# Kernel optimization log

Hardware: AMD Instinct MI355X
Metric: run time of the kernel (lower is better)

Reference implementation:

```python
import jax, jax.numpy as jnp
import numpy as np


def _maxpool3d(x, s=2):
    # MaxPool3d(kernel_size=s) -> stride=s, VALID padding
    return jax.lax.reduce_window(x, -jnp.inf, jax.lax.max,
                                 (1, 1, s, s, s), (1, 1, s, s, s), 'VALID')


def _spectral_norm(W, u):
    # W: [out_c, in_c]. One power iteration with u/v detached, matching
    # torch.nn.utils.spectral_norm's training-step behavior.
    v = W.T @ u
    v = v / (jnp.linalg.norm(v) + 1e-12)
    u2 = W @ v
    u2 = u2 / (jnp.linalg.norm(u2) + 1e-12)
    u2 = jax.lax.stop_gradient(u2)
    v = jax.lax.stop_gradient(v)
    sigma = u2 @ (W @ v)
    return W / sigma


def setup_inputs() -> dict:
    key = jax.random.key(0)
    ks = jax.random.split(key, 6)
    B, C, D = 4, 256, 32
    kc, vc, oc = 128, 128, 256
    return {
        'x':  jax.random.normal(ks[0], (B, C, D, D, D), jnp.float32),
        'Wk': jax.random.normal(ks[1], (kc, C), jnp.float32) * 0.05,  # shared f_key/f_query 1x1x1 conv
        'bk': jnp.zeros((kc,), jnp.float32),
        'Wv': jax.random.normal(ks[2], (vc, C), jnp.float32) * 0.05,  # f_value 1x1x1 conv
        'bv': jnp.zeros((vc,), jnp.float32),
        'Ww': jax.random.normal(ks[3], (oc, vc), jnp.float32) * 0.05,  # output W 1x1x1 conv
        'bw': jnp.zeros((oc,), jnp.float32),
        'u':  jax.random.normal(ks[4], (kc,), jnp.float32),            # spectral-norm power-iter vector
    }


def reference(x, Wk, bk, Wv, bv, Ww, bw, u):
    B, C = x.shape[0], x.shape[1]
    kc = Wk.shape[0]
    xp = _maxpool3d(x, 2)                      # [B,C,16,16,16]
    sp = xp.shape[2:]
    N = sp[0] * sp[1] * sp[2]                  # 4096 flattened positions
    xf = xp.reshape(B, C, N)                   # [B,C,N]

    Wq = _spectral_norm(Wk, u)                 # f_query = f_key (shared weights)
    q = jnp.einsum('kc,bcn->bnk', Wq, xf) + bk                    # [B,N,kc]
    k = jnp.einsum('kc,bcn->bkn', Wq, xf) + bk[None, :, None]     # [B,kc,N]
    v = jnp.einsum('vc,bcn->bnv', Wv, xf) + bv                    # [B,N,vc]

    sim = jnp.einsum('bnk,bkm->bnm', q, k) * (kc ** -0.5)         # [B,N,N]
    attn = jax.nn.softmax(sim, axis=-1)
    ctx = jnp.einsum('bnm,bmv->bnv', attn, v)                     # [B,N,vc]

    out = jnp.einsum('ov,bnv->bon', Ww, ctx) + bw[None, :, None]  # [B,oc,N]
    return out.reshape(B, Ww.shape[0], *sp)    # [B,oc,16,16,16] (pooled spatial, as in original)
```

## Files before the change

kernel.cpp:

```cpp
#include <hip/hip_runtime.h>

typedef __attribute__((ext_vector_type(8))) short short8;
typedef __attribute__((ext_vector_type(4))) float f32x4;

static constexpr size_t OFF_SIGMA = 0;
static constexpr size_t OFF_ML    = 256;
static constexpr size_t OFF_QKT   = 1048576;
static constexpr size_t OFF_V     = OFF_QKT + 4194304;
static constexpr size_t OFF_WCAT  = OFF_V + 4194304;
static constexpr size_t OFF_XFB   = OFF_WCAT + 196608;
static constexpr size_t OFF_PC    = OFF_XFB;

__device__ inline unsigned short f2bf(float f) {
  unsigned int u = __float_as_uint(f);
  unsigned int r = u + 0x7fffu + ((u >> 16) & 1u);
  return (unsigned short)(r >> 16);
}
__device__ inline float bf2f(unsigned short s) {
  return __uint_as_float(((unsigned int)s) << 16);
}

__launch_bounds__(256)
__global__ void k_maxpool(const float* __restrict__ x, unsigned short* __restrict__ xfb) {
  int idx = blockIdx.x * 256 + threadIdx.x;
  int n2 = idx & 2047;
  int bc = idx >> 11;
  int d2p = n2 & 7, d1 = (n2 >> 3) & 15, d0 = n2 >> 7;
  const float* p = x + (size_t)bc * 32768 + (size_t)d0 * 2048 + d1 * 64 + d2p * 4;
  float4 a = *(const float4*)(p);
  float4 b = *(const float4*)(p + 32);
  float4 c = *(const float4*)(p + 1024);
  float4 e = *(const float4*)(p + 1056);
  float o0 = fmaxf(fmaxf(fmaxf(a.x, a.y), fmaxf(b.x, b.y)),
                   fmaxf(fmaxf(c.x, c.y), fmaxf(e.x, e.y)));
  float o1 = fmaxf(fmaxf(fmaxf(a.z, a.w), fmaxf(b.z, b.w)),
                   fmaxf(fmaxf(c.z, c.w), fmaxf(e.z, e.w)));
  unsigned int pk = (unsigned int)f2bf(o0) | ((unsigned int)f2bf(o1) << 16);
  *(unsigned int*)(xfb + (size_t)bc * 4096 + n2 * 2) = pk;
}

__global__ void k_sigma(const float* __restrict__ Wk, const float* __restrict__ u,
                        float* __restrict__ sig) {
  __shared__ float vsh[256];
  __shared__ float red[256];
  __shared__ float ush[128];
  int t = threadIdx.x;
  if (t < 128) ush[t] = u[t];
  __syncthreads();
  float acc = 0.f;
  for (int k = 0; k < 128; k++) acc += Wk[(size_t)k * 256 + t] * ush[k];
  vsh[t] = acc;
  red[t] = acc * acc;
  __syncthreads();
  for (int s = 128; s > 0; s >>= 1) { if (t < s) red[t] += red[t + s]; __syncthreads(); }
  float nrm = sqrtf(red[0]) + 1e-12f;
  float vn = vsh[t] / nrm;
  __syncthreads();
  vsh[t] = vn;
  __syncthreads();
  float acc2 = 0.f;
  if (t < 128) {
    for (int c = 0; c < 256; c++) acc2 += Wk[(size_t)t * 256 + c] * vsh[c];
  }
  red[t] = (t < 128) ? acc2 * acc2 : 0.f;
  __syncthreads();
  for (int s = 128; s > 0; s >>= 1) { if (t < s) red[t] += red[t + s]; __syncthreads(); }
  if (t == 0) {
    float s2v = red[0];
    sig[0] = s2v / (sqrtf(s2v) + 1e-12f);
  }
}

__launch_bounds__(256)
__global__ void k_prep(const float* __restrict__ Ww, const float* __restrict__ Wk,
                       const float* __restrict__ Wv, unsigned short* __restrict__ wcat) {
  int i = (blockIdx.x * 256 + threadIdx.x) * 4;
  const float* src = (i < 32768) ? (Ww + i) : (i < 65536) ? (Wk + i - 32768)
                                                          : (Wv + i - 65536);
  float4 w = *(const float4*)src;
  unsigned int lo = (unsigned int)f2bf(w.x) | ((unsigned int)f2bf(w.y) << 16);
  unsigned int hi = (unsigned int)f2bf(w.z) | ((unsigned int)f2bf(w.w) << 16);
  *(uint2*)(wcat + i) = make_uint2(lo, hi);
}

__launch_bounds__(256)
__global__ void k_qkv(const unsigned short* __restrict__ xfb,
                      const unsigned short* __restrict__ wcat,
                      const float* __restrict__ bk, const float* __restrict__ bv,
                      const float* __restrict__ sig,
                      unsigned short* __restrict__ qkT, unsigned short* __restrict__ vws) {
  __shared__ __align__(16) unsigned short Bl[64 * 64];
  int bid = blockIdx.x;
  int nt = bid & 63, b = bid >> 6;
  int n0 = nt * 64;
  int t = threadIdx.x, wid = t >> 6, lane = t & 63, g = lane >> 4, lr = lane & 15;
  int R0 = wid * 64;
  bool isq = (wid < 2);
  const unsigned short* wb = isq ? (wcat + 32768 + (size_t)R0 * 256)
                                 : (wcat + 65536 + (size_t)(R0 - 128) * 256);
  f32x4 acc[4][4];
#pragma unroll
  for (int i = 0; i < 4; i++)
#pragma unroll
    for (int j = 0; j < 4; j++) acc[i][j] = (f32x4){0.f, 0.f, 0.f, 0.f};

  short8 st[2];
#pragma unroll
  for (int i = 0; i < 2; i++) {
    int gid = i * 256 + t;
    st[i] = *(const short8*)(xfb + ((size_t)(b * 256 + (gid >> 3))) * 4096 +
                             n0 + (gid & 7) * 8);
  }

#pragma unroll 1
  for (int ks4 = 0; ks4 < 4; ks4++) {
    int k0 = ks4 * 64;
    __syncthreads();
#pragma unroll
    for (int i = 0; i < 2; i++) {
      int gid = i * 256 + t;
      int c = gid >> 3, nch = gid & 7;
#pragma unroll
      for (int j = 0; j < 8; j++) {
        int n = nch * 8 + j;
        Bl[n * 64 + (((c >> 3) ^ (n & 7)) << 3) + (c & 7)] = (unsigned short)st[i][j];
      }
    }
    if (ks4 < 3) {
#pragma unroll
      for (int i = 0; i < 2; i++) {
        int gid = i * 256 + t;
        st[i] = *(const short8*)(xfb + ((size_t)(b * 256 + k0 + 64 + (gid >> 3))) * 4096 +
                                 n0 + (gid & 7) * 8);
      }
    }
    __syncthreads();
#pragma unroll
    for (int ks2 = 0; ks2 < 2; ks2++) {
      short8 af[4], bf[4];
#pragma unroll
      for (int ot = 0; ot < 4; ot++)
        af[ot] = *(const short8*)(wb + (size_t)(ot * 16 + lr) * 256 + k0 + ks2 * 32 + g * 8);
#pragma unroll
      for (int nt2 = 0; nt2 < 4; nt2++) {
        int n = nt2 * 16 + lr;
        bf[nt2] = *(const short8*)(Bl + n * 64 + (((ks2 * 4 + g) ^ (n & 7)) << 3));
      }
#pragma unroll
      for (int ot = 0; ot < 4; ot++)
#pragma unroll
        for (int nt2 = 0; nt2 < 4; nt2++)
          acc[ot][nt2] = __builtin_amdgcn_mfma_f32_16x16x32_bf16(af[ot], bf[nt2],
                                                                 acc[ot][nt2], 0, 0, 0);
    }
  }

  if (isq) {
    float inv_s = 1.0f / sig[0];
#pragma unroll
    for (int ot = 0; ot < 4; ot++)
#pragma unroll
      for (int rr = 0; rr < 4; rr++) {
        int d = R0 + ot * 16 + g * 4 + rr;
        float bias = bk[d];
#pragma unroll
        for (int nt2 = 0; nt2 < 4; nt2++) {
          int n = n0 + nt2 * 16 + lr;
          float val = acc[ot][nt2][rr] * inv_s + bias;
          int ds = ((((d >> 3) ^ (n & 7)) & 15) << 3) | (d & 7);
          qkT[((size_t)b * 4096 + n) * 128 + ds] = f2bf(val);
        }
      }
  } else {
#pragma unroll
    for (int ot = 0; ot < 4; ot++)
#pragma unroll
      for (int rr = 0; rr < 4; rr++) {
        int d = R0 - 128 + ot * 16 + g * 4 + rr;
        float bias = bv[d];
#pragma unroll
        for (int nt2 = 0; nt2 < 4; nt2++) {
          int n = n0 + nt2 * 16 + lr;
          int c = n & 63;
          int cs = ((((c >> 3) ^ (d & 7)) & 7) << 3) | (c & 7);
          vws[((size_t)(b * 128 + d)) * 4096 + (n & ~63) + cs] =
              f2bf(acc[ot][nt2][rr] + bias);
        }
      }
  }
}

__launch_bounds__(256, 2)
__global__ void k_attn(const unsigned short* __restrict__ qkT,
                       const unsigned short* __restrict__ vws,
                       unsigned short* __restrict__ pc, float* __restrict__ lsum) {
  __shared__ __align__(16) char smem[16384 + 16384 + 4 * 4608];
  const float C1 = 0.12751744f;
  int p = blockIdx.x;
  int bid = (p & 7) * 128 + (p >> 3);
  int sp = bid & 7, qt = (bid >> 3) & 31, b = bid >> 8;
  int kv0 = sp * 512;
  int t = threadIdx.x, wid = t >> 6, lane = t & 63, g = lane >> 4, lr = lane & 15;
  int qrb = qt * 128 + wid * 32;
  const unsigned short* qk_b = qkT + (size_t)b * 524288;
  const char* kgb = (const char*)qk_b;
  const char* vgb = (const char*)(vws + (size_t)b * 524288);
  char* KL = smem;
  char* VL = smem + 16384;
  unsigned short* PL = (unsigned short*)(smem + 32768 + wid * 4608);

  short8 qf[2][4];
#pragma unroll
  for (int rt = 0; rt < 2; rt++)
#pragma unroll
    for (int kk = 0; kk < 4; kk++) {
      int row = qrb + rt * 16 + lr;
      qf[rt][kk] = *(const short8*)(qk_b + (size_t)row * 128 +
                                    ((((kk * 4 + g) ^ (lr & 7)) & 15) << 3));
    }

  f32x4 cacc[2][8];
#pragma unroll
  for (int rt = 0; rt < 2; rt++)
#pragma unroll
    for (int vt = 0; vt < 8; vt++) cacc[rt][vt] = (f32x4){0.f, 0.f, 0.f, 0.f};
  float l0[4] = {0.f, 0.f, 0.f, 0.f}, l1[4] = {0.f, 0.f, 0.f, 0.f};

  int drow = t >> 3;
  int cb   = (t & 7) * 16;

  short8 kst[4], vst[4];
  {
    const char* kg = kgb + (size_t)kv0 * 256;
#pragma unroll
    for (int i = 0; i < 4; i++) kst[i] = *(const short8*)(kg + i * 4096 + t * 16);
#pragma unroll
    for (int i = 0; i < 4; i++)
      vst[i] = *(const short8*)(vgb + (size_t)(i * 32 + drow) * 8192 + kv0 * 2 + cb);
  }

#pragma unroll 1
  for (int it = 0; it < 8; ++it) {
    int mbase = kv0 + it * 64;
    __syncthreads();
#pragma unroll
    for (int i = 0; i < 4; i++) *(short8*)(KL + i * 4096 + t * 16) = kst[i];
#pragma unroll
    for (int i = 0; i < 4; i++) *(short8*)(VL + i * 4096 + t * 16) = vst[i];
    if (it < 7) {
      int mb = mbase + 64;
      const char* kg = kgb + (size_t)mb * 256;
#pragma unroll
      for (int i = 0; i < 4; i++) kst[i] = *(const short8*)(kg + i * 4096 + t * 16);
#pragma unroll
      for (int i = 0; i < 4; i++)
        vst[i] = *(const short8*)(vgb + (size_t)(i * 32 + drow) * 8192 + mb * 2 + cb);
    }
    __syncthreads();

#pragma unroll
    for (int ct = 0; ct < 4; ct++) {
      short8 kf[4];
#pragma unroll
      for (int kk = 0; kk < 4; kk++)
        kf[kk] = *(const short8*)(KL + (ct * 16 + lr) * 256 +
                                  ((((kk * 4 + g) ^ (lr & 7)) & 15) << 4));
      f32x4 a0 = {0.f, 0.f, 0.f, 0.f}, a1 = a0;
      __builtin_amdgcn_s_setprio(1);
#pragma unroll
      for (int kk = 0; kk < 4; kk++) {
        a0 = __builtin_amdgcn_mfma_f32_16x16x32_bf16(qf[0][kk], kf[kk], a0, 0, 0, 0);
        a1 = __builtin_amdgcn_mfma_f32_16x16x32_bf16(qf[1][kk], kf[kk], a1, 0, 0, 0);
      }
      __builtin_amdgcn_s_setprio(0);
#pragma unroll
      for (int r = 0; r < 4; r++) {
        float p0 = __builtin_amdgcn_exp2f(a0[r] * C1);
        float p1 = __builtin_amdgcn_exp2f(a1[r] * C1);
        l0[r] += p0;
        l1[r] += p1;
        PL[(g * 4 + r) * 72 + ct * 16 + lr] =
            (unsigned short)((__float_as_uint(p0) + 0x8000u) >> 16);
        PL[(16 + g * 4 + r) * 72 + ct * 16 + lr] =
            (unsigned short)((__float_as_uint(p1) + 0x8000u) >> 16);
      }
    }

    __builtin_amdgcn_s_setprio(1);
#pragma unroll
    for (int ks = 0; ks < 2; ks++) {
      short8 pa0 = *(const short8*)(PL + lr * 72 + ks * 32 + g * 8);
      short8 pa1 = *(const short8*)(PL + (16 + lr) * 72 + ks * 32 + g * 8);
#pragma unroll
      for (int vt = 0; vt < 8; vt++) {
        short8 vb = *(const short8*)(VL + (vt * 16 + lr) * 128 +
                                     ((((ks * 4 + g) ^ (lr & 7)) & 7) << 4));
        cacc[0][vt] = __builtin_amdgcn_mfma_f32_16x16x32_bf16(pa0, vb, cacc[0][vt], 0, 0, 0);
        cacc[1][vt] = __builtin_amdgcn_mfma_f32_16x16x32_bf16(pa1, vb, cacc[1][vt], 0, 0, 0);
      }
    }
    __builtin_amdgcn_s_setprio(0);
  }

#pragma unroll
  for (int r = 0; r < 4; r++) {
    float v = l0[r];
    v += __shfl_xor(v, 1); v += __shfl_xor(v, 2);
    v += __shfl_xor(v, 4); v += __shfl_xor(v, 8);
    l0[r] = v;
    float w = l1[r];
    w += __shfl_xor(w, 1); w += __shfl_xor(w, 2);
    w += __shfl_xor(w, 4); w += __shfl_xor(w, 8);
    l1[r] = w;
  }

  int rowrd = lane >> 4;
  int colrd = (lane & 15) * 8;
#pragma unroll
  for (int rt = 0; rt < 2; rt++) {
#pragma unroll
    for (int vt = 0; vt < 8; vt++)
#pragma unroll
      for (int r = 0; r < 4; r++)
        PL[(g * 4 + r) * 136 + vt * 16 + lr] =
            f2bf(rt ? cacc[1][vt][r] : cacc[0][vt][r]);
#pragma unroll
    for (int rnd = 0; rnd < 4; rnd++) {
      int row = rnd * 4 + rowrd;
      short8 v = *(const short8*)(PL + row * 136 + colrd);
      int n = qrb + rt * 16 + row;
      *(short8*)(pc + ((size_t)sp * 16384 + (size_t)b * 4096 + n) * 128 + colrd) = v;
    }
  }
  if (lr == 0) {
#pragma unroll
    for (int rt = 0; rt < 2; rt++)
#pragma unroll
      for (int r = 0; r < 4; r++) {
        int n = qrb + rt * 16 + g * 4 + r;
        lsum[sp * 16384 + (size_t)b * 4096 + n] = rt ? l1[r] : l0[r];
      }
  }
}

__launch_bounds__(256)
__global__ void k_mergeout(const unsigned short* __restrict__ pc,
                           const float* __restrict__ lsum,
                           const unsigned short* __restrict__ wwb,
                           const float* __restrict__ bw,
                           float* __restrict__ out) {
  __shared__ float inv_l[64];
  __shared__ __align__(16) unsigned short Bl[64 * 128];
  int bid = blockIdx.x;
  int nt = bid & 63, b = bid >> 6;
  int n0 = nt * 64;
  size_t gnb = (size_t)b * 4096 + n0;
  int t = threadIdx.x;

  if (t < 64) {
    float L = 0.f;
#pragma unroll
    for (int sp = 0; sp < 8; sp++) L += lsum[sp * 16384 + gnb + t];
    inv_l[t] = 1.f / L;
  }
  __syncthreads();

  {
    int n = t & 63, vs = t >> 6;
    float o[32] = {};
#pragma unroll
    for (int sp = 0; sp < 8; sp++) {
      const unsigned short* src = pc + ((size_t)sp * 16384 + gnb + n) * 128 + vs * 32;
#pragma unroll
      for (int c = 0; c < 4; c++) {
        short8 pv = *(const short8*)(src + c * 8);
#pragma unroll
        for (int j = 0; j < 8; j++) o[c * 8 + j] += bf2f((unsigned short)pv[j]);
      }
    }
    float inv = inv_l[n];
    unsigned int* B32 = (unsigned int*)Bl;
#pragma unroll
    for (int jj = 0; jj < 16; jj++) {
      int v = vs * 32 + jj * 2;
      int kg = v >> 3;
      int kgp = (kg & 8) | ((kg ^ n) & 7);
      unsigned int pk = (unsigned int)f2bf(o[jj * 2] * inv) |
                        ((unsigned int)f2bf(o[jj * 2 + 1] * inv) << 16);
      B32[n * 64 + kgp * 4 + ((v & 7) >> 1)] = pk;
    }
  }
  __syncthreads();

  int wid = t >> 6, lane = t & 63, g = lane >> 4, lr = lane & 15;
  int o0 = wid * 64;
  short8 af[4][4];
#pragma unroll
  for (int ot = 0; ot < 4; ot++) {
    int o = o0 + ot * 16 + lr;
#pragma unroll
    for (int ks = 0; ks < 4; ks++)
      af[ot][ks] = *(const short8*)(wwb + (size_t)o * 128 + ks * 32 + g * 8);
  }
  f32x4 acc[4][4];
#pragma unroll
  for (int i = 0; i < 4; i++)
#pragma unroll
    for (int j = 0; j < 4; j++) acc[i][j] = (f32x4){0.f, 0.f, 0.f, 0.f};
#pragma unroll
  for (int nt2 = 0; nt2 < 4; nt2++) {
    short8 bfr[4];
#pragma unroll
    for (int ks = 0; ks < 4; ks++) {
      int kg = ks * 4 + g;
      int kgp = (kg & 8) | ((kg ^ lr) & 7);
      bfr[ks] = *(const short8*)(Bl + (nt2 * 16 + lr) * 128 + kgp * 8);
    }
#pragma unroll
    for (int ot = 0; ot < 4; ot++)
#pragma unroll
      for (int ks = 0; ks < 4; ks++)
        acc[ot][nt2] = __builtin_amdgcn_mfma_f32_16x16x32_bf16(af[ot][ks], bfr[ks],
                                                               acc[ot][nt2], 0, 0, 0);
  }
#pragma unroll
  for (int ot = 0; ot < 4; ot++)
#pragma unroll
    for (int r = 0; r < 4; r++) {
      int o = o0 + ot * 16 + g * 4 + r;
      float bias = bw[o];
#pragma unroll
      for (int nt2 = 0; nt2 < 4; nt2++)
        out[((size_t)(b * 256 + o)) * 4096 + n0 + nt2 * 16 + lr] = acc[ot][nt2][r] + bias;
    }
}

extern "C" void kernel_launch(void* const* d_in, const int* in_sizes, int n_in,
                              void* d_out, int out_size, void* d_ws, size_t ws_size,
                              hipStream_t stream) {
  const float* x  = (const float*)d_in[0];
  const float* Wk = (const float*)d_in[1];
  const float* bk = (const float*)d_in[2];
  const float* Wv = (const float*)d_in[3];
  const float* bv = (const float*)d_in[4];
  const float* Ww = (const float*)d_in[5];
  const float* bw = (const float*)d_in[6];
  const float* u  = (const float*)d_in[7];

  char* ws = (char*)d_ws;
  float* sig            = (float*)(ws + OFF_SIGMA);
  float* lsum           = (float*)(ws + OFF_ML);
  unsigned short* qkT   = (unsigned short*)(ws + OFF_QKT);
  unsigned short* vbuf  = (unsigned short*)(ws + OFF_V);
  unsigned short* wcat  = (unsigned short*)(ws + OFF_WCAT);
  unsigned short* xfb   = (unsigned short*)(ws + OFF_XFB);
  unsigned short* pc    = (unsigned short*)(ws + OFF_PC);
  float* out            = (float*)d_out;

  k_maxpool<<<8192, 256, 0, stream>>>(x, xfb);
  k_sigma<<<1, 256, 0, stream>>>(Wk, u, sig);
  k_prep<<<96, 256, 0, stream>>>(Ww, Wk, Wv, wcat);
  k_qkv<<<256, 256, 0, stream>>>(xfb, wcat, bk, bv, sig, qkT, vbuf);
  k_attn<<<1024, 256, 0, stream>>>(qkT, vbuf, pc, lsum);
  k_mergeout<<<256, 256, 0, stream>>>(pc, lsum, wcat, bw, out);
}
```

Measured before the change: 107.9 us.

## Rewrite attention inner loop with 32x32 MFMA, direct LDS loads and register-resident P

The attention kernel moves from 16x16x32 to 32x32x16 bf16 MFMA and computes S transposed (K as the A operand), so the probabilities come out in registers already laid out for the PV matmul. They are packed with v_cvt_pk_bf16 and permlane32_swap, which removes the per-wave LDS round trip for P. K/V tiles are staged with global_load_lds into a double-buffered 64KB shared array, replacing the register-staged copies and one of the two barriers per iteration. The larger LDS footprint may limit occupancy, and the output layout and rounding mode change.

After: 109.6 us. No clear change (+1.6%).

```diff
diff --git a/kernel.cpp b/kernel.cpp
--- a/kernel.cpp
+++ b/kernel.cpp
@@ -2,6 +2,7 @@
 
 typedef __attribute__((ext_vector_type(8))) short short8;
 typedef __attribute__((ext_vector_type(4))) float f32x4;
+typedef __attribute__((ext_vector_type(16))) float f32x16;
 
 static constexpr size_t OFF_SIGMA = 0;
 static constexpr size_t OFF_ML    = 256;
@@ -18,6 +19,11 @@
 }
 __device__ inline float bf2f(unsigned short s) {
   return __uint_as_float(((unsigned int)s) << 16);
+}
+__device__ inline unsigned int cvtpk_bf16(float a, float b) {
+  unsigned int r;
+  asm("v_cvt_pk_bf16_f32 %0, %1, %2" : "=v"(r) : "v"(a), "v"(b));
+  return r;
 }
 
 __launch_bounds__(256)
@@ -194,153 +200,151 @@
 __global__ void k_attn(const unsigned short* __restrict__ qkT,
                        const unsigned short* __restrict__ vws,
                        unsigned short* __restrict__ pc, float* __restrict__ lsum) {
-  __shared__ __align__(16) char smem[16384 + 16384 + 4 * 4608];
+  __shared__ __align__(16) char smem[2][32768];
   const float C1 = 0.12751744f;
   int p = blockIdx.x;
   int bid = (p & 7) * 128 + (p >> 3);
   int sp = bid & 7, qt = (bid >> 3) & 31, b = bid >> 8;
   int kv0 = sp * 512;
-  int t = threadIdx.x, wid = t >> 6, lane = t & 63, g = lane >> 4, lr = lane & 15;
+  int t = threadIdx.x, wid = t >> 6, lane = t & 63;
+  int l31 = lane & 31, hi = lane >> 5;
   int qrb = qt * 128 + wid * 32;
   const unsigned short* qk_b = qkT + (size_t)b * 524288;
   const char* kgb = (const char*)qk_b;
   const char* vgb = (const char*)(vws + (size_t)b * 524288);
-  char* KL = smem;
-  char* VL = smem + 16384;
-  unsigned short* PL = (unsigned short*)(smem + 32768 + wid * 4608);
-
-  short8 qf[2][4];
-#pragma unroll
-  for (int rt = 0; rt < 2; rt++)
-#pragma unroll
-    for (int kk = 0; kk < 4; kk++) {
-      int row = qrb + rt * 16 + lr;
-      qf[rt][kk] = *(const short8*)(qk_b + (size_t)row * 128 +
-                                    ((((kk * 4 + g) ^ (lr & 7)) & 15) << 3));
-    }
-
-  f32x4 cacc[2][8];
-#pragma unroll
-  for (int rt = 0; rt < 2; rt++)
-#pragma unroll
-    for (int vt = 0; vt < 8; vt++) cacc[rt][vt] = (f32x4){0.f, 0.f, 0.f, 0.f};
-  float l0[4] = {0.f, 0.f, 0.f, 0.f}, l1[4] = {0.f, 0.f, 0.f, 0.f};
-
-  int drow = t >> 3;
-  int cb   = (t & 7) * 16;
-
-  short8 kst[4], vst[4];
+
+  bool stk = (wid < 2);
+  int ch0 = (wid & 1) * 8;
+  const char* vsrc_base = vgb + (size_t)(lane >> 3) * 8192 + (lane & 7) * 16;
+
+#define STAGE(BUF, MB)                                                         \
+  {                                                                            \
+    char* base_ = smem[BUF];                                                   \
+    _Pragma("unroll")                                                          \
+    for (int i_ = 0; i_ < 8; i_++) {                                           \
+      int ch_ = ch0 + i_;                                                      \
+      if (stk) {                                                               \
+        const char* g_ = kgb + (size_t)(MB) * 256 + ch_ * 1024 + lane * 16;    \
+        __builtin_amdgcn_global_load_lds(                                      \
+            (const __attribute__((address_space(1))) unsigned int*)g_,         \
+            (__attribute__((address_space(3))) unsigned int*)(base_ + ch_ * 1024), \
+            16, 0, 0);                                                         \
+      } else {                                                                 \
+        const char* g_ = vsrc_base + (size_t)ch_ * 65536 + (size_t)(MB) * 2;   \
+        __builtin_amdgcn_global_load_lds(                                      \
+            (const __attribute__((address_space(1))) unsigned int*)g_,         \
+            (__attribute__((address_space(3))) unsigned int*)(base_ + 16384 + ch_ * 1024), \
+            16, 0, 0);                                                         \
+      }                                                                        \
+    }                                                                          \
+  }
+
+  STAGE(0, kv0)
+
+  short8 qf[8];
   {
-    const char* kg = kgb + (size_t)kv0 * 256;
-#pragma unroll
-    for (int i = 0; i < 4; i++) kst[i] = *(const short8*)(kg + i * 4096 + t * 16);
-#pragma unroll
-    for (int i = 0; i < 4; i++)
-      vst[i] = *(const short8*)(vgb + (size_t)(i * 32 + drow) * 8192 + kv0 * 2 + cb);
-  }
+    int row = qrb + l31;
+    const unsigned short* qr = qk_b + (size_t)row * 128;
+#pragma unroll
+    for (int kk = 0; kk < 8; kk++)
+      qf[kk] = *(const short8*)(qr + (((2 * kk + hi) ^ (row & 7)) << 3));
+  }
+
+  f32x16 acc[4];
+#pragma unroll
+  for (int dt = 0; dt < 4; dt++)
+#pragma unroll
+    for (int r = 0; r < 16; r++) acc[dt][r] = 0.f;
+  float lacc = 0.f;
+
+  __syncthreads();
 
 #pragma unroll 1
   for (int it = 0; it < 8; ++it) {
-    int mbase = kv0 + it * 64;
+    int cur = it & 1;
+    if (it < 7) STAGE(cur ^ 1, kv0 + it * 64 + 64)
+    const char* KL = smem[cur];
+    const char* VL = smem[cur] + 16384;
+
+    f32x16 s0, s1;
+#pragma unroll
+    for (int r = 0; r < 16; r++) { s0[r] = 0.f; s1[r] = 0.f; }
+    __builtin_amdgcn_s_setprio(1);
+#pragma unroll
+    for (int kk = 0; kk < 8; kk++) {
+      int cs = 2 * kk + hi;
+      short8 kf0 = *(const short8*)(KL + l31 * 256 + ((cs ^ (l31 & 7)) << 4));
+      short8 kf1 = *(const short8*)(KL + (32 + l31) * 256 + ((cs ^ (l31 & 7)) << 4));
+      s0 = __builtin_amdgcn_mfma_f32_32x32x16_bf16(kf0, qf[kk], s0, 0, 0, 0);
+      s1 = __builtin_amdgcn_mfma_f32_32x32x16_bf16(kf1, qf[kk], s1, 0, 0, 0);
+    }
+    __builtin_amdgcn_s_setprio(0);
+
+    short8 pa[4];
+#pragma unroll
+    for (int ct = 0; ct < 2; ct++) {
+      unsigned int w0[4], w1[4];
+#pragma unroll
+      for (int a = 0; a < 4; a++) {
+        float v0 = ct ? s1[4 * a + 0] : s0[4 * a + 0];
+        float v1 = ct ? s1[4 * a + 1] : s0[4 * a + 1];
+        float v2 = ct ? s1[4 * a + 2] : s0[4 * a + 2];
+        float v3 = ct ? s1[4 * a + 3] : s0[4 * a + 3];
+        float p0 = __builtin_amdgcn_exp2f(v0 * C1);
+        float p1 = __builtin_amdgcn_exp2f(v1 * C1);
+        float p2 = __builtin_amdgcn_exp2f(v2 * C1);
+        float p3 = __builtin_amdgcn_exp2f(v3 * C1);
+        lacc += (p0 + p1) + (p2 + p3);
+        w0[a] = cvtpk_bf16(p0, p1);
+        w1[a] = cvtpk_bf16(p2, p3);
+      }
+#pragma unroll
+      for (int k2 = 0; k2 < 2; k2++) {
+        unsigned int xa = w0[2 * k2], ya = w0[2 * k2 + 1];
+        unsigned int xb = w1[2 * k2], yb = w1[2 * k2 + 1];
+        asm("v_permlane32_swap_b32 %0, %1" : "+v"(xa), "+v"(ya));
+        asm("v_permlane32_swap_b32 %0, %1" : "+v"(xb), "+v"(yb));
+        union { unsigned int u[4]; short8 s8; } pk_;
+        pk_.u[0] = xa; pk_.u[1] = xb; pk_.u[2] = ya; pk_.u[3] = yb;
+        pa[ct * 2 + k2] = pk_.s8;
+      }
+    }
+
+    __builtin_amdgcn_s_setprio(1);
+#pragma unroll
+    for (int ks = 0; ks < 4; ks++) {
+      int cv = 2 * ks + hi;
+#pragma unroll
+      for (int dt = 0; dt < 4; dt++) {
+        int d = dt * 32 + l31;
+        short8 vb = *(const short8*)(VL + d * 128 + ((cv ^ (d & 7)) << 4));
+        acc[dt] = __builtin_amdgcn_mfma_f32_32x32x16_bf16(pa[ks], vb, acc[dt], 0, 0, 0);
+      }
+    }
+    __builtin_amdgcn_s_setprio(0);
     __syncthreads();
-#pragma unroll
-    for (int i = 0; i < 4; i++) *(short8*)(KL + i * 4096 + t * 16) = kst[i];
-#pragma unroll
-    for (int i = 0; i < 4; i++) *(short8*)(VL + i * 4096 + t * 16) = vst[i];
-    if (it < 7) {
-      int mb = mbase + 64;
-      const char* kg = kgb + (size_t)mb * 256;
-#pragma unroll
-      for (int i = 0; i < 4; i++) kst[i] = *(const short8*)(kg + i * 4096 + t * 16);
-#pragma unroll
-      for (int i = 0; i < 4; i++)
-        vst[i] = *(const short8*)(vgb + (size_t)(i * 32 + drow) * 8192 + mb * 2 + cb);
-    }
-    __syncthreads();
-
-#pragma unroll
-    for (int ct = 0; ct < 4; ct++) {
-      short8 kf[4];
-#pragma unroll
-      for (int kk = 0; kk < 4; kk++)
-        kf[kk] = *(const short8*)(KL + (ct * 16 + lr) * 256 +
-                                  ((((kk * 4 + g) ^ (lr & 7)) & 15) << 4));
-      f32x4 a0 = {0.f, 0.f, 0.f, 0.f}, a1 = a0;
-      __builtin_amdgcn_s_setprio(1);
-#pragma unroll
-      for (int kk = 0; kk < 4; kk++) {
-        a0 = __builtin_amdgcn_mfma_f32_16x16x32_bf16(qf[0][kk], kf[kk], a0, 0, 0, 0);
-        a1 = __builtin_amdgcn_mfma_f32_16x16x32_bf16(qf[1][kk], kf[kk], a1, 0, 0, 0);
-      }
-      __builtin_amdgcn_s_setprio(0);
-#pragma unroll
-      for (int r = 0; r < 4; r++) {
-        float p0 = __builtin_amdgcn_exp2f(a0[r] * C1);
-        float p1 = __builtin_amdgcn_exp2f(a1[r] * C1);
-        l0[r] += p0;
-        l1[r] += p1;
-        PL[(g * 4 + r) * 72 + ct * 16 + lr] =
-            (unsigned short)((__float_as_uint(p0) + 0x8000u) >> 16);
-        PL[(16 + g * 4 + r) * 72 + ct * 16 + lr] =
-            (unsigned short)((__float_as_uint(p1) + 0x8000u) >> 16);
-      }
-    }
-
-    __builtin_amdgcn_s_setprio(1);
-#pragma unroll
-    for (int ks = 0; ks < 2; ks++) {
-      short8 pa0 = *(const short8*)(PL + lr * 72 + ks * 32 + g * 8);
-      short8 pa1 = *(const short8*)(PL + (16 + lr) * 72 + ks * 32 + g * 8);
-#pragma unroll
-      for (int vt = 0; vt < 8; vt++) {
-        short8 vb = *(const short8*)(VL + (vt * 16 + lr) * 128 +
-                                     ((((ks * 4 + g) ^ (lr & 7)) & 7) << 4));
-        cacc[0][vt] = __builtin_amdgcn_mfma_f32_16x16x32_bf16(pa0, vb, cacc[0][vt], 0, 0, 0);
-        cacc[1][vt] = __builtin_amdgcn_mfma_f32_16x16x32_bf16(pa1, vb, cacc[1][vt], 0, 0, 0);
-      }
-    }
-    __builtin_amdgcn_s_setprio(0);
-  }
-
-#pragma unroll
-  for (int r = 0; r < 4; r++) {
-    float v = l0[r];
-    v += __shfl_xor(v, 1); v += __shfl_xor(v, 2);
-    v += __shfl_xor(v, 4); v += __shfl_xor(v, 8);
-    l0[r] = v;
-    float w = l1[r];
-    w += __shfl_xor(w, 1); w += __shfl_xor(w, 2);
-    w += __shfl_xor(w, 4); w += __shfl_xor(w, 8);
-    l1[r] = w;
-  }
-
-  int rowrd = lane >> 4;
-  int colrd = (lane & 15) * 8;
-#pragma unroll
-  for (int rt = 0; rt < 2; rt++) {
-#pragma unroll
-    for (int vt = 0; vt < 8; vt++)
-#pragma unroll
-      for (int r = 0; r < 4; r++)
-        PL[(g * 4 + r) * 136 + vt * 16 + lr] =
-            f2bf(rt ? cacc[1][vt][r] : cacc[0][vt][r]);
-#pragma unroll
-    for (int rnd = 0; rnd < 4; rnd++) {
-      int row = rnd * 4 + rowrd;
-      short8 v = *(const short8*)(PL + row * 136 + colrd);
-      int n = qrb + rt * 16 + row;
-      *(short8*)(pc + ((size_t)sp * 16384 + (size_t)b * 4096 + n) * 128 + colrd) = v;
-    }
-  }
-  if (lr == 0) {
-#pragma unroll
-    for (int rt = 0; rt < 2; rt++)
-#pragma unroll
-      for (int r = 0; r < 4; r++) {
-        int n = qrb + rt * 16 + g * 4 + r;
-        lsum[sp * 16384 + (size_t)b * 4096 + n] = rt ? l1[r] : l0[r];
-      }
-  }
+  }
+
+  float lf = lacc + __shfl_xor(lacc, 32);
+
+  char* OL = smem[0] + wid * 8704;
+#pragma unroll
+  for (int dt = 0; dt < 4; dt++)
+#pragma unroll
+    for (int r = 0; r < 16; r++) {
+      int q = (r & 3) + 8 * (r >> 2) + 4 * hi;
+      *(unsigned short*)(OL + q * 272 + (dt * 32 + l31) * 2) = f2bf(acc[dt][r]);
+    }
+  unsigned short* dst = pc + ((size_t)sp * 16384 + (size_t)b * 4096 + qrb) * 128;
+#pragma unroll
+  for (int j = 0; j < 8; j++) {
+    int row = lane >> 1;
+    int off = (lane & 1) * 128 + j * 16;
+    short8 v = *(const short8*)(OL + row * 272 + off);
+    *(short8*)((char*)dst + row * 256 + off) = v;
+  }
+  if (lane < 32) lsum[sp * 16384 + (size_t)b * 4096 + qrb + l31] = lf;
+#undef STAGE
 }
 
 __launch_bounds__(256)
```
